# Kernel optimization log

Hardware: AMD Instinct MI355X
Metric: run time of the kernel (lower is better)

## Reference

```python
import jax, jax.numpy as jnp
import numpy as np

B, T, D = 64, 128, 1024
E = 2048      # embedding_dim of state encoder
CD = 256      # VQ code_dim
NC = 1024     # num_codes
BETA = 0.25   # commitment cost


def setup_inputs() -> dict:
    key = jax.random.key(0)
    ks = jax.random.split(key, 5)
    states = jax.random.normal(ks[0], (B, T, D), dtype=jnp.float32)
    next_states = jax.random.normal(ks[1], (B, T, D), dtype=jnp.float32)
    # VarianceScaling(scale=2.0, fan_in) init
    W_s = jax.random.normal(ks[2], (D, E), dtype=jnp.float32) * np.sqrt(2.0 / D)
    b_s = jnp.zeros((E,), dtype=jnp.float32)
    W_p = jax.random.normal(ks[3], (2 * E, CD), dtype=jnp.float32) * np.sqrt(2.0 / (2 * E))
    b_p = jnp.zeros((CD,), dtype=jnp.float32)
    codebook = jax.random.normal(ks[4], (NC, CD), dtype=jnp.float32)
    return {"states": states, "next_states": next_states, "W_s": W_s,
            "b_s": b_s, "W_p": W_p, "b_p": b_p, "codebook": codebook}


def reference(states, next_states, W_s, b_s, W_p, b_p, codebook):
    # dual state encoder (shared weights)
    se = states @ W_s + b_s            # (B,T,E)
    ne = next_states @ W_s + b_s       # (B,T,E)
    policy_input = jax.nn.gelu(jnp.concatenate([se, ne], axis=-1))  # (B,T,2E)
    latent = policy_input @ W_p + b_p  # (B,T,CD)

    # --- VectorQuantizerEMA forward ---
    flat = latent.reshape(-1, CD)      # (N, CD), N = B*T
    # squared euclidean distances to codebook rows
    dists = (jnp.sum(flat * flat, axis=1, keepdims=True)
             - 2.0 * flat @ codebook.T
             + jnp.sum(codebook * codebook, axis=1))  # (N, NC)
    idx = jnp.argmin(dists, axis=1)                    # (N,)
    encodings = jax.nn.one_hot(idx, NC, dtype=latent.dtype)  # (N, NC)
    quantize = codebook[idx].reshape(latent.shape)     # (B,T,CD)

    e_latent_loss = jnp.mean(jnp.square(jax.lax.stop_gradient(quantize) - latent))
    loss = BETA * e_latent_loss
    # straight-through estimator
    quantize_st = latent + jax.lax.stop_gradient(quantize - latent)

    avg_probs = jnp.mean(encodings, axis=0)
    perplexity = jnp.exp(-jnp.sum(avg_probs * jnp.log(avg_probs + 1e-10)))

    encodings = encodings.reshape(B, T, NC)
    encoding_indices = idx.reshape(B, T)
    return quantize_st, loss, perplexity, encodings, encoding_indices
```

## Files before the change

kernel.cpp:

```cpp
#include <hip/hip_runtime.h>

#define NROW  8192
#define D_    1024
#define E_    2048
#define P2E_  4096
#define CD_   256
#define NC_   1024
#define BETA_ 0.25f

typedef __attribute__((ext_vector_type(8))) short short8;
typedef __attribute__((ext_vector_type(4))) float f32x4;

__device__ __forceinline__ ushort f2bf(float x) {
    union { float f; unsigned u; } v; v.f = x;
    unsigned r = (v.u + 0x7fffu + ((v.u >> 16) & 1u)) >> 16;
    return (ushort)r;
}
__device__ __forceinline__ float bf2f(ushort h) {
    union { unsigned u; float f; } v; v.u = ((unsigned)h) << 16;
    return v.f;
}
__device__ __forceinline__ void split2(float x, ushort& h, ushort& l) {
    h = f2bf(x);
    l = f2bf(x - bf2f(h));
}
__device__ __forceinline__ float gelu_tanh(float x) {
    float x3 = x * x * x;
    return 0.5f * x * (1.0f + tanhf(0.7978845608028654f * (x + 0.044715f * x3)));
}

#define GLD16(gp, lp) __builtin_amdgcn_global_load_lds( \
    (const __attribute__((address_space(1))) void*)(gp), \
    (__attribute__((address_space(3))) void*)(lp), 16, 0, 0)

template<int EPI>
__global__ __launch_bounds__(256)
void gemm_bf16x3(const ushort* __restrict__ Ah, const ushort* __restrict__ Al,
                 const ushort* __restrict__ Bh, const ushort* __restrict__ Bl,
                 int K, int ksteps,
                 const float* __restrict__ bias,
                 float* __restrict__ outF,
                 ushort* __restrict__ oPh, ushort* __restrict__ oPl,
                 const float* __restrict__ rn, const float* __restrict__ cn)
{
    __shared__ alignas(16) ushort sAh[4096], sAl[4096], sBh[4096], sBl[4096];
    const int t = threadIdx.x;
    const int l = t & 63;
    const int w = t >> 6;
    const int wr = w >> 1, wc = w & 1;

    const int nxy = gridDim.x * gridDim.y;
    const int id  = blockIdx.y * gridDim.x + blockIdx.x;
    const int swz = (id & 7) * (nxy >> 3) + (id >> 3);
    const int bx  = swz % gridDim.x;
    const int by  = swz / gridDim.x;

    const int bm = by * 128;
    const int bn = bx * 128;
    const int kstart = (EPI == 1) ? (int)blockIdx.z * (ksteps * 32) : 0;

    const int srow = t >> 2;
    const int scol = ((t & 3) ^ ((t >> 3) & 3)) * 8;
    const ushort* gAh = Ah + (size_t)(bm + srow) * K + kstart + scol;
    const ushort* gAl = Al + (size_t)(bm + srow) * K + kstart + scol;
    const ushort* gBh = Bh + (size_t)(bn + srow) * K + kstart + scol;
    const ushort* gBl = Bl + (size_t)(bn + srow) * K + kstart + scol;
    const size_t rstep = (size_t)64 * K;
    const int lo0 = t * 8, lo1 = t * 8 + 2048;

    f32x4 acc[4][4];
#pragma unroll
    for (int i = 0; i < 4; i++)
#pragma unroll
        for (int j = 0; j < 4; j++) acc[i][j] = (f32x4)0.0f;

    const int rsw = ((l >> 4) ^ (((l & 15) >> 1) & 3)) * 8;
    const int ar = (wr * 64 + (l & 15)) * 32 + rsw;
    const int br = (wc * 64 + (l & 15)) * 32 + rsw;

#define STAGE8() do { \
        GLD16(gAh, &sAh[lo0]); GLD16(gAh + rstep, &sAh[lo1]); \
        GLD16(gAl, &sAl[lo0]); GLD16(gAl + rstep, &sAl[lo1]); \
        GLD16(gBh, &sBh[lo0]); GLD16(gBh + rstep, &sBh[lo1]); \
        GLD16(gBl, &sBl[lo0]); GLD16(gBl + rstep, &sBl[lo1]); \
    } while (0)

    STAGE8();
    __syncthreads();

    for (int s = 0; s < ksteps; ++s) {
        short8 fah[4], fal[4], fbh[4], fbl[4];
#pragma unroll
        for (int i = 0; i < 4; i++) {
            fah[i] = *(const short8*)&sAh[ar + i * 16 * 32];
            fal[i] = *(const short8*)&sAl[ar + i * 16 * 32];
            fbh[i] = *(const short8*)&sBh[br + i * 16 * 32];
            fbl[i] = *(const short8*)&sBl[br + i * 16 * 32];
        }
        __syncthreads();

        if (s + 1 < ksteps) {
            gAh += 32; gAl += 32; gBh += 32; gBl += 32;
            STAGE8();
        }

        __builtin_amdgcn_s_setprio(1);
#pragma unroll
        for (int i = 0; i < 4; i++)
#pragma unroll
            for (int j = 0; j < 4; j++) {
                acc[i][j] = __builtin_amdgcn_mfma_f32_16x16x32_bf16(fah[i], fbh[j], acc[i][j], 0, 0, 0);
                acc[i][j] = __builtin_amdgcn_mfma_f32_16x16x32_bf16(fah[i], fbl[j], acc[i][j], 0, 0, 0);
                acc[i][j] = __builtin_amdgcn_mfma_f32_16x16x32_bf16(fal[i], fbh[j], acc[i][j], 0, 0, 0);
            }
        __builtin_amdgcn_s_setprio(0);
        __syncthreads();
    }
#undef STAGE8

#pragma unroll
    for (int i = 0; i < 4; i++) {
        const int grow = bm + wr * 64 + i * 16 + (l >> 4) * 4;
#pragma unroll
        for (int j = 0; j < 4; j++) {
            const int gcol = bn + wc * 64 + j * 16 + (l & 15);
            f32x4 a = acc[i][j];
            if constexpr (EPI == 0) {
                const float bb = bias[gcol];
#pragma unroll
                for (int r = 0; r < 4; r++) {
                    int m = grow + r;
                    float x = gelu_tanh(a[r] + bb);
                    ushort h, lo; split2(x, h, lo);
                    int pr = (m < NROW) ? m : m - NROW;
                    int pc = ((m < NROW) ? 0 : E_) + gcol;
                    oPh[(size_t)pr * P2E_ + pc] = h;
                    oPl[(size_t)pr * P2E_ + pc] = lo;
                }
            } else if constexpr (EPI == 1) {
                float* o = outF + ((size_t)NROW * blockIdx.z + grow) * CD_ + gcol;
#pragma unroll
                for (int r = 0; r < 4; r++) o[(size_t)r * CD_] = a[r];
            } else {
#pragma unroll
                for (int r = 0; r < 4; r++) {
                    int m = grow + r;
                    outF[(size_t)m * NC_ + gcol] = (rn[m] - 2.0f * a[r]) + cn[gcol];
                }
            }
        }
    }
}

__global__ void split_k(const float* __restrict__ in, ushort* __restrict__ oh,
                        ushort* __restrict__ ol, int n4)
{
    int i = blockIdx.x * blockDim.x + threadIdx.x;
    int stride = gridDim.x * blockDim.x;
    for (; i < n4; i += stride) {
        float4 v = ((const float4*)in)[i];
        ushort4 h, lo;
        split2(v.x, h.x, lo.x); split2(v.y, h.y, lo.y);
        split2(v.z, h.z, lo.z); split2(v.w, h.w, lo.w);
        ((ushort4*)oh)[i] = h;
        ((ushort4*)ol)[i] = lo;
    }
}

__global__ __launch_bounds__(1024)
void tsplit_k(const float* __restrict__ in, ushort* __restrict__ oh,
              ushort* __restrict__ ol, int R, int C)
{
    __shared__ float tile[32][33];
    int c0 = blockIdx.x * 32, r0 = blockIdx.y * 32;
    int tx = threadIdx.x, ty = threadIdx.y;
    tile[ty][tx] = in[(size_t)(r0 + ty) * C + c0 + tx];
    __syncthreads();
    float x = tile[tx][ty];
    ushort h, lo; split2(x, h, lo);
    size_t o = (size_t)(c0 + ty) * R + r0 + tx;
    oh[o] = h; ol[o] = lo;
}

__global__ __launch_bounds__(256)
void combine_k(const float* __restrict__ part, const float* __restrict__ bias,
               float* __restrict__ latent, ushort* __restrict__ lh,
               ushort* __restrict__ ll, float* __restrict__ rown)
{
    __shared__ float red[256];
    int row = blockIdx.x, t = threadIdx.x;
    float x = bias[t];
#pragma unroll
    for (int z = 0; z < 4; z++) x += part[((size_t)z * NROW + row) * CD_ + t];
    latent[(size_t)row * CD_ + t] = x;
    ushort h, lo; split2(x, h, lo);
    lh[(size_t)row * CD_ + t] = h;
    ll[(size_t)row * CD_ + t] = lo;
    red[t] = x * x;
    __syncthreads();
    for (int st = 128; st > 0; st >>= 1) { if (t < st) red[t] += red[t + st]; __syncthreads(); }
    if (t == 0) rown[row] = red[0];
}

__global__ __launch_bounds__(256) void row_norms(const float* __restrict__ X,
                                                 float* __restrict__ out)
{
    __shared__ float s[256];
    int n = blockIdx.x, t = threadIdx.x;
    float v = X[(size_t)n * 256 + t];
    s[t] = v * v;
    __syncthreads();
    for (int st = 128; st > 0; st >>= 1) {
        if (t < st) s[t] += s[t + st];
        __syncthreads();
    }
    if (t == 0) out[n] = s[0];
}

__global__ void zero_hist(int* hist) { hist[threadIdx.x] = 0; }

__global__ __launch_bounds__(256) void vq_kernel(
    const float* __restrict__ latent, const float* __restrict__ cb,
    float* __restrict__ dists_enc, float* __restrict__ out_q,
    float* __restrict__ out_idx, int* __restrict__ hist, float* __restrict__ lpart)
{
    __shared__ float sd[256];
    __shared__ int   si[256];
    const int n = blockIdx.x, tid = threadIdx.x;
    float* drow = dists_enc + (size_t)n * NC_;

    float best = INFINITY;
    int bidx = 0;
#pragma unroll
    for (int j = 0; j < NC_ / 256; j++) {
        int c = tid + j * 256;
        float d = drow[c];
        if (d < best) { best = d; bidx = c; }
    }
    sd[tid] = best; si[tid] = bidx;
    __syncthreads();
    for (int st = 128; st > 0; st >>= 1) {
        if (tid < st) {
            float d2 = sd[tid + st]; int i2 = si[tid + st];
            if (d2 < sd[tid] || (d2 == sd[tid] && i2 < si[tid])) { sd[tid] = d2; si[tid] = i2; }
        }
        __syncthreads();
    }
    const int bc = si[0];

#pragma unroll
    for (int j = 0; j < NC_ / 256; j++) {
        int c = tid + j * 256;
        drow[c] = (c == bc) ? 1.0f : 0.0f;
    }

    float lv = latent[(size_t)n * CD_ + tid];
    float q  = cb[(size_t)bc * CD_ + tid];
    out_q[(size_t)n * CD_ + tid] = lv + (q - lv);
    float diff = q - lv;
    __syncthreads();
    sd[tid] = diff * diff;
    __syncthreads();
    for (int st = 128; st > 0; st >>= 1) {
        if (tid < st) sd[tid] += sd[tid + st];
        __syncthreads();
    }
    if (tid == 0) {
        lpart[n] = sd[0];
        atomicAdd(&hist[bc], 1);
        out_idx[n] = (float)bc;
    }
}

__global__ __launch_bounds__(1024) void finalize_kernel(
    const float* __restrict__ lpart, const int* __restrict__ hist,
    float* __restrict__ out_loss, float* __restrict__ out_perp)
{
    __shared__ float s[1024];
    int t = threadIdx.x;
    float x = 0.0f;
    for (int i = t; i < NROW; i += 1024) x += lpart[i];
    s[t] = x;
    __syncthreads();
    for (int st = 512; st > 0; st >>= 1) {
        if (t < st) s[t] += s[t + st];
        __syncthreads();
    }
    float total = s[0];
    __syncthreads();
    float p = (float)hist[t] * (1.0f / NROW);
    s[t] = p * logf(p + 1e-10f);
    __syncthreads();
    for (int st = 512; st > 0; st >>= 1) {
        if (t < st) s[t] += s[t + st];
        __syncthreads();
    }
    if (t == 0) {
        *out_loss = BETA_ * (total / (float)((size_t)NROW * CD_));
        *out_perp = expf(-s[0]);
    }
}

extern "C" void kernel_launch(void* const* d_in, const int* in_sizes, int n_in,
                              void* d_out, int out_size, void* d_ws, size_t ws_size,
                              hipStream_t stream)
{
    const float* states      = (const float*)d_in[0];
    const float* next_states = (const float*)d_in[1];
    const float* W_s         = (const float*)d_in[2];
    const float* b_s         = (const float*)d_in[3];
    const float* W_p         = (const float*)d_in[4];
    const float* b_p         = (const float*)d_in[5];
    const float* codebook    = (const float*)d_in[6];

    float* out      = (float*)d_out;
    float* out_q    = out;
    float* out_loss = out + (size_t)NROW * CD_;
    float* out_perp = out_loss + 1;
    float* out_enc  = out_perp + 1;
    float* out_idx  = out_enc + (size_t)NROW * NC_;

    char* ws = (char*)d_ws;
    size_t off = 0;
    auto alloc = [&](size_t bytes) { void* p = ws + off; off += (bytes + 255) & ~255ull; return p; };

    ushort* A1h  = (ushort*)alloc((size_t)2 * NROW * D_ * 2);
    ushort* A1l  = (ushort*)alloc((size_t)2 * NROW * D_ * 2);
    ushort* WsTh = (ushort*)alloc((size_t)E_ * D_ * 2);
    ushort* WsTl = (ushort*)alloc((size_t)E_ * D_ * 2);
    ushort* WpTh = (ushort*)alloc((size_t)CD_ * P2E_ * 2);
    ushort* WpTl = (ushort*)alloc((size_t)CD_ * P2E_ * 2);
    ushort* cbh  = (ushort*)alloc((size_t)NC_ * CD_ * 2);
    ushort* cbl  = (ushort*)alloc((size_t)NC_ * CD_ * 2);
    ushort* Ph   = (ushort*)alloc((size_t)NROW * P2E_ * 2);
    ushort* Pl   = (ushort*)alloc((size_t)NROW * P2E_ * 2);
    ushort* lath = (ushort*)alloc((size_t)NROW * CD_ * 2);
    ushort* latl = (ushort*)alloc((size_t)NROW * CD_ * 2);
    float*  rown = (float*)alloc(NROW * 4);
    float*  cbn  = (float*)alloc(NC_ * 4);
    int*    hist = (int*)alloc(NC_ * 4);
    float*  lpart= (float*)alloc(NROW * 4);
    float* lat_part = (float*)A1h;
    float* latent   = (float*)WsTh;

    {
        int n4 = NROW * D_ / 4;
        split_k<<<2048, 256, 0, stream>>>(states, A1h, A1l, n4);
        split_k<<<2048, 256, 0, stream>>>(next_states, A1h + (size_t)NROW * D_,
                                          A1l + (size_t)NROW * D_, n4);
    }
    tsplit_k<<<dim3(E_ / 32, D_ / 32), dim3(32, 32), 0, stream>>>(W_s, WsTh, WsTl, D_, E_);
    tsplit_k<<<dim3(CD_ / 32, P2E_ / 32), dim3(32, 32), 0, stream>>>(W_p, WpTh, WpTl, P2E_, CD_);
    split_k<<<256, 256, 0, stream>>>(codebook, cbh, cbl, NC_ * CD_ / 4);
    row_norms<<<NC_, 256, 0, stream>>>(codebook, cbn);

    gemm_bf16x3<0><<<dim3(E_ / 128, 2 * NROW / 128), 256, 0, stream>>>(
        A1h, A1l, WsTh, WsTl, D_, D_ / 32, b_s, nullptr, Ph, Pl, nullptr, nullptr);

    gemm_bf16x3<1><<<dim3(CD_ / 128, NROW / 128, 4), 256, 0, stream>>>(
        Ph, Pl, WpTh, WpTl, P2E_, P2E_ / 32 / 4, nullptr, lat_part, nullptr, nullptr, nullptr, nullptr);

    combine_k<<<NROW, 256, 0, stream>>>(lat_part, b_p, latent, lath, latl, rown);

    gemm_bf16x3<2><<<dim3(NC_ / 128, NROW / 128), 256, 0, stream>>>(
        lath, latl, cbh, cbl, CD_, CD_ / 32, nullptr, out_enc, nullptr, nullptr, rown, cbn);

    zero_hist<<<1, NC_, 0, stream>>>(hist);
    vq_kernel<<<NROW, 256, 0, stream>>>(latent, codebook, out_enc, out_q, out_idx, hist, lpart);
    finalize_kernel<<<1, 1024, 0, stream>>>(lpart, hist, out_loss, out_perp);
}
```

Baseline: 346.2 us.

## Fuse argmin into distance GEMM, double-buffer LDS, raise split-K to 8

The distance GEMM epilogue now computes a per-block argmin (dropping the row-norm term, which does not change the argmin) and writes zeros to the encodings, so the full distance matrix is no longer written and then re-read by the VQ kernel. A small vq2 kernel merges the 8 per-column-block candidates and sets the single one-hot entry. Separately, the GEMM main loop uses double-buffered LDS so the next tile's loads overlap compute, and the second GEMM's split-K factor goes from 4 to 8. Double buffering doubles LDS use per block, which may lower occupancy.

Result: slower. 378.8 us (+9.4%).

```diff
diff --git a/kernel.cpp b/kernel.cpp
--- a/kernel.cpp
+++ b/kernel.cpp
@@ -7,6 +7,7 @@
 #define CD_   256
 #define NC_   1024
 #define BETA_ 0.25f
+#define SPLITK 8
 
 typedef __attribute__((ext_vector_type(8))) short short8;
 typedef __attribute__((ext_vector_type(4))) float f32x4;
@@ -41,9 +42,12 @@
                  const float* __restrict__ bias,
                  float* __restrict__ outF,
                  ushort* __restrict__ oPh, ushort* __restrict__ oPl,
-                 const float* __restrict__ rn, const float* __restrict__ cn)
-{
-    __shared__ alignas(16) ushort sAh[4096], sAl[4096], sBh[4096], sBl[4096];
+                 const float* __restrict__ cn,
+                 float* __restrict__ candv, int* __restrict__ candi)
+{
+    __shared__ alignas(16) ushort sAh[2][4096], sAl[2][4096], sBh[2][4096], sBl[2][4096];
+    __shared__ float redv[128][2];
+    __shared__ int   redi[128][2];
     const int t = threadIdx.x;
     const int l = t & 63;
     const int w = t >> 6;
@@ -78,32 +82,30 @@
     const int ar = (wr * 64 + (l & 15)) * 32 + rsw;
     const int br = (wc * 64 + (l & 15)) * 32 + rsw;
 
-#define STAGE8() do { \
-        GLD16(gAh, &sAh[lo0]); GLD16(gAh + rstep, &sAh[lo1]); \
-        GLD16(gAl, &sAl[lo0]); GLD16(gAl + rstep, &sAl[lo1]); \
-        GLD16(gBh, &sBh[lo0]); GLD16(gBh + rstep, &sBh[lo1]); \
-        GLD16(gBl, &sBl[lo0]); GLD16(gBl + rstep, &sBl[lo1]); \
+#define STAGE8(b) do { \
+        GLD16(gAh, &sAh[b][lo0]); GLD16(gAh + rstep, &sAh[b][lo1]); \
+        GLD16(gAl, &sAl[b][lo0]); GLD16(gAl + rstep, &sAl[b][lo1]); \
+        GLD16(gBh, &sBh[b][lo0]); GLD16(gBh + rstep, &sBh[b][lo1]); \
+        GLD16(gBl, &sBl[b][lo0]); GLD16(gBl + rstep, &sBl[b][lo1]); \
     } while (0)
 
-    STAGE8();
+    STAGE8(0);
     __syncthreads();
 
     for (int s = 0; s < ksteps; ++s) {
-        short8 fah[4], fal[4], fbh[4], fbl[4];
-#pragma unroll
-        for (int i = 0; i < 4; i++) {
-            fah[i] = *(const short8*)&sAh[ar + i * 16 * 32];
-            fal[i] = *(const short8*)&sAl[ar + i * 16 * 32];
-            fbh[i] = *(const short8*)&sBh[br + i * 16 * 32];
-            fbl[i] = *(const short8*)&sBl[br + i * 16 * 32];
-        }
-        __syncthreads();
-
+        const int cb_ = s & 1;
         if (s + 1 < ksteps) {
             gAh += 32; gAl += 32; gBh += 32; gBl += 32;
-            STAGE8();
-        }
-
+            STAGE8(cb_ ^ 1);
+        }
+        short8 fah[4], fal[4], fbh[4], fbl[4];
+#pragma unroll
+        for (int i = 0; i < 4; i++) {
+            fah[i] = *(const short8*)&sAh[cb_][ar + i * 16 * 32];
+            fal[i] = *(const short8*)&sAl[cb_][ar + i * 16 * 32];
+            fbh[i] = *(const short8*)&sBh[cb_][br + i * 16 * 32];
+            fbl[i] = *(const short8*)&sBl[cb_][br + i * 16 * 32];
+        }
         __builtin_amdgcn_s_setprio(1);
 #pragma unroll
         for (int i = 0; i < 4; i++)
@@ -117,6 +119,46 @@
         __syncthreads();
     }
 #undef STAGE8
+
+    if constexpr (EPI == 2) {
+        float cnv[4];
+#pragma unroll
+        for (int j = 0; j < 4; j++) cnv[j] = cn[bn + wc * 64 + j * 16 + (l & 15)];
+#pragma unroll
+        for (int i = 0; i < 4; i++) {
+            const int grow = bm + wr * 64 + i * 16 + (l >> 4) * 4;
+#pragma unroll
+            for (int r = 0; r < 4; r++) {
+                float bv = INFINITY; int bi = 0;
+#pragma unroll
+                for (int j = 0; j < 4; j++) {
+                    float d = cnv[j] - 2.0f * acc[i][j][r];
+                    int c = bn + wc * 64 + j * 16 + (l & 15);
+                    if (d < bv) { bv = d; bi = c; }
+                }
+#pragma unroll
+                for (int m = 1; m < 16; m <<= 1) {
+                    float ov = __shfl_xor(bv, m, 64);
+                    int   oi = __shfl_xor(bi, m, 64);
+                    if (ov < bv || (ov == bv && oi < bi)) { bv = ov; bi = oi; }
+                }
+                int rl = wr * 64 + i * 16 + (l >> 4) * 4 + r;
+                if ((l & 15) == 0) { redv[rl][wc] = bv; redi[rl][wc] = bi; }
+#pragma unroll
+                for (int j = 0; j < 4; j++)
+                    outF[(size_t)(grow + r) * NC_ + bn + wc * 64 + j * 16 + (l & 15)] = 0.0f;
+            }
+        }
+        __syncthreads();
+        if (t < 128) {
+            float v0 = redv[t][0], v1 = redv[t][1];
+            int   i0 = redi[t][0], i1 = redi[t][1];
+            bool take1 = (v1 < v0) || (v1 == v0 && i1 < i0);
+            candv[(size_t)(bm + t) * 8 + bx] = take1 ? v1 : v0;
+            candi[(size_t)(bm + t) * 8 + bx] = take1 ? i1 : i0;
+        }
+        return;
+    }
 
 #pragma unroll
     for (int i = 0; i < 4; i++) {
@@ -141,12 +183,6 @@
                 float* o = outF + ((size_t)NROW * blockIdx.z + grow) * CD_ + gcol;
 #pragma unroll
                 for (int r = 0; r < 4; r++) o[(size_t)r * CD_] = a[r];
-            } else {
-#pragma unroll
-                for (int r = 0; r < 4; r++) {
-                    int m = grow + r;
-                    outF[(size_t)m * NC_ + gcol] = (rn[m] - 2.0f * a[r]) + cn[gcol];
-                }
             }
         }
     }
@@ -185,21 +221,16 @@
 __global__ __launch_bounds__(256)
 void combine_k(const float* __restrict__ part, const float* __restrict__ bias,
                float* __restrict__ latent, ushort* __restrict__ lh,
-               ushort* __restrict__ ll, float* __restrict__ rown)
-{
-    __shared__ float red[256];
+               ushort* __restrict__ ll)
+{
     int row = blockIdx.x, t = threadIdx.x;
     float x = bias[t];
 #pragma unroll
-    for (int z = 0; z < 4; z++) x += part[((size_t)z * NROW + row) * CD_ + t];
+    for (int z = 0; z < SPLITK; z++) x += part[((size_t)z * NROW + row) * CD_ + t];
     latent[(size_t)row * CD_ + t] = x;
     ushort h, lo; split2(x, h, lo);
     lh[(size_t)row * CD_ + t] = h;
     ll[(size_t)row * CD_ + t] = lo;
-    red[t] = x * x;
-    __syncthreads();
-    for (int st = 128; st > 0; st >>= 1) { if (t < st) red[t] += red[t + st]; __syncthreads(); }
-    if (t == 0) rown[row] = red[0];
 }
 
 __global__ __launch_bounds__(256) void row_norms(const float* __restrict__ X,
@@ -219,53 +250,41 @@
 
 __global__ void zero_hist(int* hist) { hist[threadIdx.x] = 0; }
 
-__global__ __launch_bounds__(256) void vq_kernel(
+__global__ __launch_bounds__(256) void vq2_kernel(
     const float* __restrict__ latent, const float* __restrict__ cb,
-    float* __restrict__ dists_enc, float* __restrict__ out_q,
+    const float* __restrict__ candv, const int* __restrict__ candi,
+    float* __restrict__ out_enc, float* __restrict__ out_q,
     float* __restrict__ out_idx, int* __restrict__ hist, float* __restrict__ lpart)
 {
     __shared__ float sd[256];
-    __shared__ int   si[256];
-    const int n = blockIdx.x, tid = threadIdx.x;
-    float* drow = dists_enc + (size_t)n * NC_;
-
-    float best = INFINITY;
-    int bidx = 0;
-#pragma unroll
-    for (int j = 0; j < NC_ / 256; j++) {
-        int c = tid + j * 256;
-        float d = drow[c];
-        if (d < best) { best = d; bidx = c; }
-    }
-    sd[tid] = best; si[tid] = bidx;
+    __shared__ int sbc;
+    const int n = blockIdx.x, t = threadIdx.x;
+    if (t == 0) {
+        const float* cv = candv + (size_t)n * 8;
+        const int*   ci = candi + (size_t)n * 8;
+        float bv = cv[0]; int bi = ci[0];
+#pragma unroll
+        for (int k = 1; k < 8; k++) {
+            float v = cv[k]; int x = ci[k];
+            if (v < bv || (v == bv && x < bi)) { bv = v; bi = x; }
+        }
+        sbc = bi;
+    }
+    __syncthreads();
+    const int bc = sbc;
+    if (t == 0) out_enc[(size_t)n * NC_ + bc] = 1.0f;
+
+    float lv = latent[(size_t)n * CD_ + t];
+    float q  = cb[(size_t)bc * CD_ + t];
+    out_q[(size_t)n * CD_ + t] = lv + (q - lv);
+    float diff = q - lv;
+    sd[t] = diff * diff;
     __syncthreads();
     for (int st = 128; st > 0; st >>= 1) {
-        if (tid < st) {
-            float d2 = sd[tid + st]; int i2 = si[tid + st];
-            if (d2 < sd[tid] || (d2 == sd[tid] && i2 < si[tid])) { sd[tid] = d2; si[tid] = i2; }
-        }
-        __syncthreads();
-    }
-    const int bc = si[0];
-
-#pragma unroll
-    for (int j = 0; j < NC_ / 256; j++) {
-        int c = tid + j * 256;
-        drow[c] = (c == bc) ? 1.0f : 0.0f;
-    }
-
-    float lv = latent[(size_t)n * CD_ + tid];
-    float q  = cb[(size_t)bc * CD_ + tid];
-    out_q[(size_t)n * CD_ + tid] = lv + (q - lv);
-    float diff = q - lv;
-    __syncthreads();
-    sd[tid] = diff * diff;
-    __syncthreads();
-    for (int st = 128; st > 0; st >>= 1) {
-        if (tid < st) sd[tid] += sd[tid + st];
-        __syncthreads();
-    }
-    if (tid == 0) {
+        if (t < st) sd[t] += sd[t + st];
+        __syncthreads();
+    }
+    if (t == 0) {
         lpart[n] = sd[0];
         atomicAdd(&hist[bc], 1);
         out_idx[n] = (float)bc;
@@ -336,10 +355,11 @@
     ushort* Pl   = (ushort*)alloc((size_t)NROW * P2E_ * 2);
     ushort* lath = (ushort*)alloc((size_t)NROW * CD_ * 2);
     ushort* latl = (ushort*)alloc((size_t)NROW * CD_ * 2);
-    float*  rown = (float*)alloc(NROW * 4);
     float*  cbn  = (float*)alloc(NC_ * 4);
     int*    hist = (int*)alloc(NC_ * 4);
     float*  lpart= (float*)alloc(NROW * 4);
+    float*  candv= (float*)alloc((size_t)NROW * 8 * 4);
+    int*    candi= (int*)alloc((size_t)NROW * 8 * 4);
     float* lat_part = (float*)A1h;
     float* latent   = (float*)WsTh;
 
@@ -355,17 +375,20 @@
     row_norms<<<NC_, 256, 0, stream>>>(codebook, cbn);
 
     gemm_bf16x3<0><<<dim3(E_ / 128, 2 * NROW / 128), 256, 0, stream>>>(
-        A1h, A1l, WsTh, WsTl, D_, D_ / 32, b_s, nullptr, Ph, Pl, nullptr, nullptr);
-
-    gemm_bf16x3<1><<<dim3(CD_ / 128, NROW / 128, 4), 256, 0, stream>>>(
-        Ph, Pl, WpTh, WpTl, P2E_, P2E_ / 32 / 4, nullptr, lat_part, nullptr, nullptr, nullptr, nullptr);
-
-    combine_k<<<NROW, 256, 0, stream>>>(lat_part, b_p, latent, lath, latl, rown);
+        A1h, A1l, WsTh, WsTl, D_, D_ / 32, b_s, nullptr, Ph, Pl, nullptr, nullptr, nullptr);
+
+    gemm_bf16x3<1><<<dim3(CD_ / 128, NROW / 128, SPLITK), 256, 0, stream>>>(
+        Ph, Pl, WpTh, WpTl, P2E_, P2E_ / 32 / SPLITK, nullptr, lat_part, nullptr, nullptr,
+        nullptr, nullptr, nullptr);
+
+    combine_k<<<NROW, 256, 0, stream>>>(lat_part, b_p, latent, lath, latl);
 
     gemm_bf16x3<2><<<dim3(NC_ / 128, NROW / 128), 256, 0, stream>>>(
-        lath, latl, cbh, cbl, CD_, CD_ / 32, nullptr, out_enc, nullptr, nullptr, rown, cbn);
+        lath, latl, cbh, cbl, CD_, CD_ / 32, nullptr, out_enc, nullptr, nullptr,
+        cbn, candv, candi);
 
     zero_hist<<<1, NC_, 0, stream>>>(hist);
-    vq_kernel<<<NROW, 256, 0, stream>>>(latent, codebook, out_enc, out_q, out_idx, hist, lpart);
+    vq2_kernel<<<NROW, 256, 0, stream>>>(latent, codebook, candv, candi,
+                                         out_enc, out_q, out_idx, hist, lpart);
     finalize_kernel<<<1, 1024, 0, stream>>>(lpart, hist, out_loss, out_perp);
 }
```

## Double-buffer LDS in bf16x3 GEMM with explicit vmcnt waits and prefetch-two

Applied to the files above, without the earlier changes.

Turns the shared GEMM's single LDS buffer into a double buffer. It prefetches two k-steps ahead and uses explicit s_waitcnt vmcnt plus s_barrier in place of __syncthreads, so global-to-LDS loads overlap with the MFMA work. It also restructures fragment loads so A fragments are read per row-tile inside the MFMA loop, which cuts register pressure, and adds launch_bounds(256,2) to target two blocks per CU. LDS use doubles to 64KB per block, and the hand-counted vmcnt ordering is fragile.

New measurement: 368.8 us. 1.07x slower.

```diff
diff --git a/kernel.cpp b/kernel.cpp
--- a/kernel.cpp
+++ b/kernel.cpp
@@ -7,6 +7,7 @@
 #define CD_   256
 #define NC_   1024
 #define BETA_ 0.25f
+#define SPLITK 4
 
 typedef __attribute__((ext_vector_type(8))) short short8;
 typedef __attribute__((ext_vector_type(4))) float f32x4;
@@ -34,7 +35,7 @@
     (__attribute__((address_space(3))) void*)(lp), 16, 0, 0)
 
 template<int EPI>
-__global__ __launch_bounds__(256)
+__global__ __launch_bounds__(256, 2)
 void gemm_bf16x3(const ushort* __restrict__ Ah, const ushort* __restrict__ Al,
                  const ushort* __restrict__ Bh, const ushort* __restrict__ Bl,
                  int K, int ksteps,
@@ -43,7 +44,7 @@
                  ushort* __restrict__ oPh, ushort* __restrict__ oPl,
                  const float* __restrict__ rn, const float* __restrict__ cn)
 {
-    __shared__ alignas(16) ushort sAh[4096], sAl[4096], sBh[4096], sBl[4096];
+    __shared__ alignas(16) ushort sAh[2][4096], sAl[2][4096], sBh[2][4096], sBl[2][4096];
     const int t = threadIdx.x;
     const int l = t & 63;
     const int w = t >> 6;
@@ -74,56 +75,57 @@
 #pragma unroll
         for (int j = 0; j < 4; j++) acc[i][j] = (f32x4)0.0f;
 
-    const int rsw = ((l >> 4) ^ (((l & 15) >> 1) & 3)) * 8;
-    const int ar = (wr * 64 + (l & 15)) * 32 + rsw;
-    const int br = (wc * 64 + (l & 15)) * 32 + rsw;
-
-#define STAGE8() do { \
-        GLD16(gAh, &sAh[lo0]); GLD16(gAh + rstep, &sAh[lo1]); \
-        GLD16(gAl, &sAl[lo0]); GLD16(gAl + rstep, &sAl[lo1]); \
-        GLD16(gBh, &sBh[lo0]); GLD16(gBh + rstep, &sBh[lo1]); \
-        GLD16(gBl, &sBl[lo0]); GLD16(gBl + rstep, &sBl[lo1]); \
+    const int kq = l >> 4, lr = l & 15;
+    const int rsw = (kq ^ ((lr >> 1) & 3)) * 8;
+    const int ar = (wr * 64 + lr) * 32 + rsw;
+    const int br = (wc * 64 + lr) * 32 + rsw;
+
+#define STG(buf, koff) do { \
+        GLD16(gAh + (koff), &sAh[buf][lo0]); GLD16(gAh + (koff) + rstep, &sAh[buf][lo1]); \
+        GLD16(gAl + (koff), &sAl[buf][lo0]); GLD16(gAl + (koff) + rstep, &sAl[buf][lo1]); \
+        GLD16(gBh + (koff), &sBh[buf][lo0]); GLD16(gBh + (koff) + rstep, &sBh[buf][lo1]); \
+        GLD16(gBl + (koff), &sBl[buf][lo0]); GLD16(gBl + (koff) + rstep, &sBl[buf][lo1]); \
     } while (0)
 
-    STAGE8();
-    __syncthreads();
+    STG(0, 0);
+    STG(1, 32);
 
     for (int s = 0; s < ksteps; ++s) {
-        short8 fah[4], fal[4], fbh[4], fbl[4];
+        const int cur = s & 1;
+        if (s + 1 < ksteps) asm volatile("s_waitcnt vmcnt(8)" ::: "memory");
+        else                asm volatile("s_waitcnt vmcnt(0)" ::: "memory");
+        asm volatile("s_barrier" ::: "memory");
+
+        short8 fbh[4], fbl[4];
+#pragma unroll
+        for (int j = 0; j < 4; j++) {
+            fbh[j] = *(const short8*)&sBh[cur][br + j * 512];
+            fbl[j] = *(const short8*)&sBl[cur][br + j * 512];
+        }
+        __builtin_amdgcn_s_setprio(1);
 #pragma unroll
         for (int i = 0; i < 4; i++) {
-            fah[i] = *(const short8*)&sAh[ar + i * 16 * 32];
-            fal[i] = *(const short8*)&sAl[ar + i * 16 * 32];
-            fbh[i] = *(const short8*)&sBh[br + i * 16 * 32];
-            fbl[i] = *(const short8*)&sBl[br + i * 16 * 32];
+            short8 fah = *(const short8*)&sAh[cur][ar + i * 512];
+            short8 fal = *(const short8*)&sAl[cur][ar + i * 512];
+#pragma unroll
+            for (int j = 0; j < 4; j++) {
+                acc[i][j] = __builtin_amdgcn_mfma_f32_16x16x32_bf16(fah, fbh[j], acc[i][j], 0, 0, 0);
+                acc[i][j] = __builtin_amdgcn_mfma_f32_16x16x32_bf16(fah, fbl[j], acc[i][j], 0, 0, 0);
+                acc[i][j] = __builtin_amdgcn_mfma_f32_16x16x32_bf16(fal, fbh[j], acc[i][j], 0, 0, 0);
+            }
         }
-        __syncthreads();
-
-        if (s + 1 < ksteps) {
-            gAh += 32; gAl += 32; gBh += 32; gBl += 32;
-            STAGE8();
-        }
-
-        __builtin_amdgcn_s_setprio(1);
-#pragma unroll
-        for (int i = 0; i < 4; i++)
-#pragma unroll
-            for (int j = 0; j < 4; j++) {
-                acc[i][j] = __builtin_amdgcn_mfma_f32_16x16x32_bf16(fah[i], fbh[j], acc[i][j], 0, 0, 0);
-                acc[i][j] = __builtin_amdgcn_mfma_f32_16x16x32_bf16(fah[i], fbl[j], acc[i][j], 0, 0, 0);
-                acc[i][j] = __builtin_amdgcn_mfma_f32_16x16x32_bf16(fal[i], fbh[j], acc[i][j], 0, 0, 0);
-            }
         __builtin_amdgcn_s_setprio(0);
-        __syncthreads();
-    }
-#undef STAGE8
+        asm volatile("s_barrier" ::: "memory");
+        if (s + 2 < ksteps) STG(cur, (s + 2) * 32);
+    }
+#undef STG
 
 #pragma unroll
     for (int i = 0; i < 4; i++) {
-        const int grow = bm + wr * 64 + i * 16 + (l >> 4) * 4;
+        const int grow = bm + wr * 64 + i * 16 + kq * 4;
 #pragma unroll
         for (int j = 0; j < 4; j++) {
-            const int gcol = bn + wc * 64 + j * 16 + (l & 15);
+            const int gcol = bn + wc * 64 + j * 16 + lr;
             f32x4 a = acc[i][j];
             if constexpr (EPI == 0) {
                 const float bb = bias[gcol];
@@ -191,7 +193,7 @@
     int row = blockIdx.x, t = threadIdx.x;
     float x = bias[t];
 #pragma unroll
-    for (int z = 0; z < 4; z++) x += part[((size_t)z * NROW + row) * CD_ + t];
+    for (int z = 0; z < SPLITK; z++) x += part[((size_t)z * NROW + row) * CD_ + t];
     latent[(size_t)row * CD_ + t] = x;
     ushort h, lo; split2(x, h, lo);
     lh[(size_t)row * CD_ + t] = h;
@@ -357,15 +359,18 @@
     gemm_bf16x3<0><<<dim3(E_ / 128, 2 * NROW / 128), 256, 0, stream>>>(
         A1h, A1l, WsTh, WsTl, D_, D_ / 32, b_s, nullptr, Ph, Pl, nullptr, nullptr);
 
-    gemm_bf16x3<1><<<dim3(CD_ / 128, NROW / 128, 4), 256, 0, stream>>>(
-        Ph, Pl, WpTh, WpTl, P2E_, P2E_ / 32 / 4, nullptr, lat_part, nullptr, nullptr, nullptr, nullptr);
+    gemm_bf16x3<1><<<dim3(CD_ / 128, NROW / 128, SPLITK), 256, 0, stream>>>(
+        Ph, Pl, WpTh, WpTl, P2E_, P2E_ / 32 / SPLITK, nullptr, lat_part, nullptr, nullptr,
+        nullptr, nullptr);
 
     combine_k<<<NROW, 256, 0, stream>>>(lat_part, b_p, latent, lath, latl, rown);
 
     gemm_bf16x3<2><<<dim3(NC_ / 128, NROW / 128), 256, 0, stream>>>(
-        lath, latl, cbh, cbl, CD_, CD_ / 32, nullptr, out_enc, nullptr, nullptr, rown, cbn);
+        lath, latl, cbh, cbl, CD_, CD_ / 32, nullptr, out_enc, nullptr, nullptr,
+        rown, cbn);
 
     zero_hist<<<1, NC_, 0, stream>>>(hist);
     vq_kernel<<<NROW, 256, 0, stream>>>(latent, codebook, out_enc, out_q, out_idx, hist, lpart);
+
     finalize_kernel<<<1, 1024, 0, stream>>>(lpart, hist, out_loss, out_perp);
 }
```
